# Performance work log

Measured on AMD Instinct MI355X. Metric: run time of the kernel, lower is better.

Reference implementation:

```python
import jax, jax.numpy as jnp
import numpy as np

NUM_CAPSULE = 10
DIM_CAPSULE = 16
NUM_ROUTING = 3
EPS = 1e-7  # tf.keras.backend.epsilon()


def squash(v, axis=-1):
    s2 = jnp.sum(jnp.square(v), axis=axis, keepdims=True)
    scale = s2 / (1.0 + s2) / jnp.sqrt(s2 + EPS)
    return scale * v


def setup_inputs() -> dict:
    key = jax.random.key(0)
    k1, k2 = jax.random.split(key)
    B, in_dim = 16384, 2048
    inputs = jax.random.normal(k1, (B, in_dim), dtype=jnp.float32)
    # glorot-uniform-ish scale for the kernel
    limit = np.sqrt(6.0 / (in_dim + NUM_CAPSULE * DIM_CAPSULE)).astype(np.float32)
    kernel = jax.random.uniform(k2, (in_dim, NUM_CAPSULE * DIM_CAPSULE),
                                dtype=jnp.float32, minval=-limit, maxval=limit)
    return {"inputs": inputs, "kernel": kernel}


def reference(inputs, kernel):
    B = inputs.shape[0]
    # [B, in_dim] @ [in_dim, nc*dc] -> [B, nc, dc]
    inputs_hat = (inputs @ kernel).reshape(B, NUM_CAPSULE, DIM_CAPSULE)
    b = jnp.zeros((B, NUM_CAPSULE, 1), dtype=inputs.dtype)
    outputs = None
    for _ in range(NUM_ROUTING):
        c = jax.nn.softmax(b, axis=1)                      # [B, nc, 1]
        s = jnp.sum(c * inputs_hat, axis=1, keepdims=True)  # [B, 1, dc]
        outputs = squash(s)                                 # [B, 1, dc]
        # matmul(inputs_hat, outputs, transpose_b=True) -> [B, nc, 1]
        b = b + jnp.einsum('bnd,bd->bn', inputs_hat, outputs[:, 0, :])[:, :, None]
    return outputs[:, 0, :]  # [B, dc]
```

## Files before the change

kernel.cpp:

```cpp
#include <hip/hip_runtime.h>

typedef unsigned int u32;
typedef unsigned short u16;
typedef __attribute__((ext_vector_type(8))) __bf16 bf16x8;
typedef __attribute__((ext_vector_type(4))) float f32x4;

#define N_CAP 10
#define D_CAP 16
#define NN 160
#define KK 2048
#define BM 64
#define NSTEPS 64
#define THREADS 704
#define HAT_STRIDE 165
#define BSTEP 20480
#define ATILE 8192
#define NBUF 4

__device__ __align__(16) unsigned char Wpack_g[NSTEPS * BSTEP];

__device__ __forceinline__ u32 pack_hi(float f0, float f1) {
  return __builtin_amdgcn_perm(__builtin_bit_cast(u32, f1),
                               __builtin_bit_cast(u32, f0), 0x07060302u);
}
__device__ __forceinline__ float hi_part(float f) {
  u32 u = __builtin_bit_cast(u32, f) & 0xFFFF0000u;
  return __builtin_bit_cast(float, u);
}
union U4B8 { uint4 u; bf16x8 b; };

__device__ __forceinline__ void split2(const float4& x, const float4& y,
                                       bf16x8& h, bf16x8& l) {
  U4B8 hh, ll;
  hh.u.x = pack_hi(x.x, x.y); hh.u.y = pack_hi(x.z, x.w);
  hh.u.z = pack_hi(y.x, y.y); hh.u.w = pack_hi(y.z, y.w);
  float l0 = x.x - hi_part(x.x), l1 = x.y - hi_part(x.y);
  float l2 = x.z - hi_part(x.z), l3 = x.w - hi_part(x.w);
  float l4 = y.x - hi_part(y.x), l5 = y.y - hi_part(y.y);
  float l6 = y.z - hi_part(y.z), l7 = y.w - hi_part(y.w);
  ll.u.x = pack_hi(l0, l1); ll.u.y = pack_hi(l2, l3);
  ll.u.z = pack_hi(l4, l5); ll.u.w = pack_hi(l6, l7);
  h = hh.b; l = ll.b;
}

__device__ __forceinline__ void mfma12(bf16x8 ah0, bf16x8 al0, bf16x8 ah1,
                                       bf16x8 al1, bf16x8 bh0, bf16x8 bh1,
                                       bf16x8 bl0, bf16x8 bl1, f32x4& a00,
                                       f32x4& a01, f32x4& a10, f32x4& a11) {
  a00 = __builtin_amdgcn_mfma_f32_16x16x32_bf16(ah0, bh0, a00, 0, 0, 0);
  a00 = __builtin_amdgcn_mfma_f32_16x16x32_bf16(ah0, bl0, a00, 0, 0, 0);
  a00 = __builtin_amdgcn_mfma_f32_16x16x32_bf16(al0, bh0, a00, 0, 0, 0);
  a01 = __builtin_amdgcn_mfma_f32_16x16x32_bf16(ah0, bh1, a01, 0, 0, 0);
  a01 = __builtin_amdgcn_mfma_f32_16x16x32_bf16(ah0, bl1, a01, 0, 0, 0);
  a01 = __builtin_amdgcn_mfma_f32_16x16x32_bf16(al0, bh1, a01, 0, 0, 0);
  a10 = __builtin_amdgcn_mfma_f32_16x16x32_bf16(ah1, bh0, a10, 0, 0, 0);
  a10 = __builtin_amdgcn_mfma_f32_16x16x32_bf16(ah1, bl0, a10, 0, 0, 0);
  a10 = __builtin_amdgcn_mfma_f32_16x16x32_bf16(al1, bh0, a10, 0, 0, 0);
  a11 = __builtin_amdgcn_mfma_f32_16x16x32_bf16(ah1, bh1, a11, 0, 0, 0);
  a11 = __builtin_amdgcn_mfma_f32_16x16x32_bf16(ah1, bl1, a11, 0, 0, 0);
  a11 = __builtin_amdgcn_mfma_f32_16x16x32_bf16(al1, bh1, a11, 0, 0, 0);
}

__global__ void pack_w(const float* __restrict__ W) {
  const int tid = blockIdx.x * 256 + threadIdx.x;
  if (tid >= NSTEPS * 4 * 5 * 64) return;
  const int lane = tid & 63;
  const int rest = tid >> 6;
  const int wjp = rest % 5;
  const int rest2 = rest / 5;
  const int v = rest2 & 3;
  const int s = rest2 >> 2;
  const int col = 32 * wjp + 16 * (v & 1) + (lane & 15);
  const int kb = 32 * s + 8 * (lane >> 4);
  u32 r[4];
#pragma unroll
  for (int jj = 0; jj < 4; ++jj) {
    float x0 = W[(size_t)(kb + 2 * jj) * NN + col];
    float x1 = W[(size_t)(kb + 2 * jj + 1) * NN + col];
    if (v >= 2) { x0 -= hi_part(x0); x1 -= hi_part(x1); }
    r[jj] = pack_hi(x0, x1);
  }
  uint4 o; o.x = r[0]; o.y = r[1]; o.z = r[2]; o.w = r[3];
  *(uint4*)(Wpack_g + (size_t)tid * 16) = o;
}

#define GLOAD(gp, lp) __builtin_amdgcn_global_load_lds( \
    (const __attribute__((address_space(1))) u32*)(gp), \
    (__attribute__((address_space(3))) u32*)(lp), 16, 0, 0)
#define BARRIER() asm volatile("s_barrier" ::: "memory")

__global__ __launch_bounds__(THREADS, 1) void capsule_fused(
    const float* __restrict__ X, float* __restrict__ out) {
  __shared__ __align__(16) char AsA[NBUF * ATILE];
  __shared__ __align__(16) char AsB[NBUF * BSTEP];
  __shared__ __align__(16) float hat[BM * HAT_STRIDE];

  const int t = threadIdx.x;
  const int rbase = blockIdx.x * BM;
  const int lane = t & 63;
  const int w = t >> 6;

  if (w == 10) {
    const float* g0 = X + (size_t)(rbase + (lane >> 3)) * KK
                        + (size_t)(((lane & 7) ^ (lane >> 3)) * 4);
    const unsigned char* gw0 = Wpack_g + (size_t)lane * 16;
#define STAGE(S, BV) do {                                         \
    const float* ga_ = g0 + (size_t)(S) * 32;                     \
    char* la_ = AsA + (BV) * ATILE;                               \
    GLOAD(ga_,           la_);                                    \
    GLOAD(ga_ +  8 * KK, la_ + 1024);                             \
    GLOAD(ga_ + 16 * KK, la_ + 2048);                             \
    GLOAD(ga_ + 24 * KK, la_ + 3072);                             \
    GLOAD(ga_ + 32 * KK, la_ + 4096);                             \
    GLOAD(ga_ + 40 * KK, la_ + 5120);                             \
    GLOAD(ga_ + 48 * KK, la_ + 6144);                             \
    GLOAD(ga_ + 56 * KK, la_ + 7168);                             \
    const unsigned char* gw_ = gw0 + (size_t)(S) * BSTEP;         \
    char* lw_ = AsB + (BV) * BSTEP;                               \
    _Pragma("unroll")                                             \
    for (int c_ = 0; c_ < 20; ++c_)                               \
      GLOAD(gw_ + c_ * 1024, lw_ + c_ * 1024);                    \
  } while (0)
    STAGE(0, 0);
    STAGE(1, 1);
    asm volatile("s_waitcnt vmcnt(0)" ::: "memory");
    BARRIER();
    STAGE(2, 2);
    BARRIER();
#pragma unroll 1
    for (int i = 0; i < NSTEPS; ++i) {
      if (i + 3 < NSTEPS) {
        STAGE(i + 3, (i + 3) & 3);
        asm volatile("s_waitcnt vmcnt(28)" ::: "memory");
      } else {
        asm volatile("s_waitcnt vmcnt(0)" ::: "memory");
      }
      BARRIER();
    }
#undef STAGE
  } else {
    const int wip = (w >= 5) ? 1 : 0;
    const int wjp = w - 5 * wip;
    const int l15 = lane & 15;
    const int q = lane >> 4;
    const int r0 = 32 * wip + l15;
    const int r1 = r0 + 16;
    const int c0 = 2 * q, c1 = 2 * q + 1;
    const int o00 = (r0 >> 3) * 1024 + (r0 & 7) * 128 + ((c0 ^ (r0 & 7)) << 4);
    const int o01 = (r0 >> 3) * 1024 + (r0 & 7) * 128 + ((c1 ^ (r0 & 7)) << 4);
    const int o10 = (r1 >> 3) * 1024 + (r1 & 7) * 128 + ((c0 ^ (r1 & 7)) << 4);
    const int o11 = (r1 >> 3) * 1024 + (r1 & 7) * 128 + ((c1 ^ (r1 & 7)) << 4);
    const int ob = wjp * 1024 + lane * 16;

    f32x4 acc00 = {0.f,0.f,0.f,0.f}, acc01 = {0.f,0.f,0.f,0.f};
    f32x4 acc10 = {0.f,0.f,0.f,0.f}, acc11 = {0.f,0.f,0.f,0.f};

    float4 A00a, A01a, A10a, A11a, A00b, A01b, A10b, A11b;
    bf16x8 Bh0a, Bh1a, Bl0a, Bl1a, Bh0b, Bh1b, Bl0b, Bl1b;

#define READSET(SFX, SLOT) do {                                   \
    const char* ca_ = AsA + (SLOT) * ATILE;                       \
    const char* cb_ = AsB + (SLOT) * BSTEP + ob;                  \
    A00##SFX = *(const float4*)(ca_ + o00);                       \
    A01##SFX = *(const float4*)(ca_ + o01);                       \
    A10##SFX = *(const float4*)(ca_ + o10);                       \
    A11##SFX = *(const float4*)(ca_ + o11);                       \
    Bh0##SFX = *(const bf16x8*)(cb_);                             \
    Bh1##SFX = *(const bf16x8*)(cb_ + 5120);                      \
    Bl0##SFX = *(const bf16x8*)(cb_ + 10240);                     \
    Bl1##SFX = *(const bf16x8*)(cb_ + 15360);                     \
  } while (0)

#define COMPUTE(SFX) do {                                         \
    bf16x8 ah0, al0, ah1, al1;                                    \
    split2(A00##SFX, A01##SFX, ah0, al0);                         \
    split2(A10##SFX, A11##SFX, ah1, al1);                         \
    __builtin_amdgcn_s_setprio(1);                                \
    mfma12(ah0, al0, ah1, al1, Bh0##SFX, Bh1##SFX, Bl0##SFX,      \
           Bl1##SFX, acc00, acc01, acc10, acc11);                 \
    __builtin_amdgcn_s_setprio(0);                                \
  } while (0)

    BARRIER();
    READSET(a, 0);
    BARRIER();
    int ni = 1;
#pragma unroll 1
    for (int ii = 0; ii < NSTEPS / 2; ++ii) {
      READSET(b, ni);
      ni = (ni + 1) & 3;
      COMPUTE(a);
      BARRIER();
      if (ii != NSTEPS / 2 - 1) {
        READSET(a, ni);
        ni = (ni + 1) & 3;
      }
      COMPUTE(b);
      BARRIER();
    }
#undef READSET
#undef COMPUTE

#pragma unroll
    for (int r = 0; r < 4; ++r) {
      const int rowb = 32 * wip + 4 * q + r;
      const int colb = 32 * wjp + l15;
      hat[rowb * HAT_STRIDE + colb]             = acc00[r];
      hat[rowb * HAT_STRIDE + colb + 16]        = acc01[r];
      hat[(rowb + 16) * HAT_STRIDE + colb]      = acc10[r];
      hat[(rowb + 16) * HAT_STRIDE + colb + 16] = acc11[r];
    }
  }
  __syncthreads();

  if (t < BM * 8) {
    const int r = t >> 3;
    const int d0 = t & 7;
    float h0[N_CAP], h1[N_CAP];
#pragma unroll
    for (int n = 0; n < N_CAP; ++n) {
      h0[n] = hat[r * HAT_STRIDE + n * D_CAP + d0];
      h1[n] = hat[r * HAT_STRIDE + n * D_CAP + d0 + 8];
    }
    float bb[N_CAP];
#pragma unroll
    for (int n = 0; n < N_CAP; ++n) bb[n] = 0.f;
    float v0 = 0.f, v1 = 0.f;
#pragma unroll
    for (int it = 0; it < 3; ++it) {
      float mx = bb[0];
#pragma unroll
      for (int n = 1; n < N_CAP; ++n) mx = fmaxf(mx, bb[n]);
      float c[N_CAP], se = 0.f;
#pragma unroll
      for (int n = 0; n < N_CAP; ++n) { c[n] = __expf(bb[n] - mx); se += c[n]; }
      const float inv = 1.f / se;
      float s0 = 0.f, s1 = 0.f;
#pragma unroll
      for (int n = 0; n < N_CAP; ++n) { s0 += c[n] * h0[n]; s1 += c[n] * h1[n]; }
      s0 *= inv; s1 *= inv;
      float s2 = s0 * s0 + s1 * s1;
      s2 += __shfl_xor(s2, 1);
      s2 += __shfl_xor(s2, 2);
      s2 += __shfl_xor(s2, 4);
      const float scale = s2 / ((1.f + s2) * sqrtf(s2 + 1e-7f));
      v0 = scale * s0; v1 = scale * s1;
      if (it < 2) {
#pragma unroll
        for (int n = 0; n < N_CAP; ++n) {
          float dd = h0[n] * v0 + h1[n] * v1;
          dd += __shfl_xor(dd, 1);
          dd += __shfl_xor(dd, 2);
          dd += __shfl_xor(dd, 4);
          bb[n] += dd;
        }
      }
    }
    out[(size_t)(rbase + r) * D_CAP + d0] = v0;
    out[(size_t)(rbase + r) * D_CAP + d0 + 8] = v1;
  }
}

extern "C" void kernel_launch(void* const* d_in, const int* in_sizes, int n_in,
                              void* d_out, int out_size, void* d_ws, size_t ws_size,
                              hipStream_t stream) {
  const float* X = (const float*)d_in[0];
  const float* W = (const float*)d_in[1];
  if (n_in >= 2 && in_sizes[0] == KK * NN) {
    X = (const float*)d_in[1];
    W = (const float*)d_in[0];
  }
  (void)d_ws; (void)ws_size; (void)out_size;
  pack_w<<<(NSTEPS * 4 * 5 * 64 + 255) / 256, 256, 0, stream>>>(W);
  capsule_fused<<<16384 / BM, THREADS, 0, stream>>>(X, (float*)d_out);
}
```

Measured before the change: 202.1 us.

## Load packed weight fragments directly from global into registers, dropping LDS staging

The packed bf16 hi/lo weight tiles are no longer staged through LDS by the loader wave. Each compute wave now reads its 64-byte per-lane fragment straight from global memory (L2-resident) with a one-step register prefetch. The pack layout is reordered so each lane's four fragments are contiguous, and the loader's vmcnt wait drops to match fewer in-flight loads. This frees about 80KB of LDS and shrinks loader traffic, but exposes compute waves to global-load latency and adds vector registers.

```diff
diff --git a/kernel.cpp b/kernel.cpp
--- a/kernel.cpp
+++ b/kernel.cpp
@@ -44,32 +44,33 @@
 }
 
 __device__ __forceinline__ void mfma12(bf16x8 ah0, bf16x8 al0, bf16x8 ah1,
-                                       bf16x8 al1, bf16x8 bh0, bf16x8 bh1,
-                                       bf16x8 bl0, bf16x8 bl1, f32x4& a00,
-                                       f32x4& a01, f32x4& a10, f32x4& a11) {
-  a00 = __builtin_amdgcn_mfma_f32_16x16x32_bf16(ah0, bh0, a00, 0, 0, 0);
-  a00 = __builtin_amdgcn_mfma_f32_16x16x32_bf16(ah0, bl0, a00, 0, 0, 0);
-  a00 = __builtin_amdgcn_mfma_f32_16x16x32_bf16(al0, bh0, a00, 0, 0, 0);
-  a01 = __builtin_amdgcn_mfma_f32_16x16x32_bf16(ah0, bh1, a01, 0, 0, 0);
-  a01 = __builtin_amdgcn_mfma_f32_16x16x32_bf16(ah0, bl1, a01, 0, 0, 0);
-  a01 = __builtin_amdgcn_mfma_f32_16x16x32_bf16(al0, bh1, a01, 0, 0, 0);
-  a10 = __builtin_amdgcn_mfma_f32_16x16x32_bf16(ah1, bh0, a10, 0, 0, 0);
-  a10 = __builtin_amdgcn_mfma_f32_16x16x32_bf16(ah1, bl0, a10, 0, 0, 0);
-  a10 = __builtin_amdgcn_mfma_f32_16x16x32_bf16(al1, bh0, a10, 0, 0, 0);
-  a11 = __builtin_amdgcn_mfma_f32_16x16x32_bf16(ah1, bh1, a11, 0, 0, 0);
-  a11 = __builtin_amdgcn_mfma_f32_16x16x32_bf16(ah1, bl1, a11, 0, 0, 0);
-  a11 = __builtin_amdgcn_mfma_f32_16x16x32_bf16(al1, bh1, a11, 0, 0, 0);
+                                       bf16x8 al1, uint4 b0, uint4 b1, uint4 b2,
+                                       uint4 b3, f32x4& a00, f32x4& a01,
+                                       f32x4& a10, f32x4& a11) {
+  U4B8 u0, u1, u2, u3;
+  u0.u = b0; u1.u = b1; u2.u = b2; u3.u = b3;
+  a00 = __builtin_amdgcn_mfma_f32_16x16x32_bf16(ah0, u0.b, a00, 0, 0, 0);
+  a00 = __builtin_amdgcn_mfma_f32_16x16x32_bf16(ah0, u2.b, a00, 0, 0, 0);
+  a00 = __builtin_amdgcn_mfma_f32_16x16x32_bf16(al0, u0.b, a00, 0, 0, 0);
+  a01 = __builtin_amdgcn_mfma_f32_16x16x32_bf16(ah0, u1.b, a01, 0, 0, 0);
+  a01 = __builtin_amdgcn_mfma_f32_16x16x32_bf16(ah0, u3.b, a01, 0, 0, 0);
+  a01 = __builtin_amdgcn_mfma_f32_16x16x32_bf16(al0, u1.b, a01, 0, 0, 0);
+  a10 = __builtin_amdgcn_mfma_f32_16x16x32_bf16(ah1, u0.b, a10, 0, 0, 0);
+  a10 = __builtin_amdgcn_mfma_f32_16x16x32_bf16(ah1, u2.b, a10, 0, 0, 0);
+  a10 = __builtin_amdgcn_mfma_f32_16x16x32_bf16(al1, u0.b, a10, 0, 0, 0);
+  a11 = __builtin_amdgcn_mfma_f32_16x16x32_bf16(ah1, u1.b, a11, 0, 0, 0);
+  a11 = __builtin_amdgcn_mfma_f32_16x16x32_bf16(ah1, u3.b, a11, 0, 0, 0);
+  a11 = __builtin_amdgcn_mfma_f32_16x16x32_bf16(al1, u1.b, a11, 0, 0, 0);
 }
 
 __global__ void pack_w(const float* __restrict__ W) {
   const int tid = blockIdx.x * 256 + threadIdx.x;
-  if (tid >= NSTEPS * 4 * 5 * 64) return;
-  const int lane = tid & 63;
-  const int rest = tid >> 6;
-  const int wjp = rest % 5;
-  const int rest2 = rest / 5;
-  const int v = rest2 & 3;
-  const int s = rest2 >> 2;
+  if (tid >= NSTEPS * 5 * 64 * 4) return;
+  const int v = tid & 3;
+  const int lane = (tid >> 2) & 63;
+  const int sw = tid >> 8;
+  const int wjp = sw % 5;
+  const int s = sw / 5;
   const int col = 32 * wjp + 16 * (v & 1) + (lane & 15);
   const int kb = 32 * s + 8 * (lane >> 4);
   u32 r[4];
@@ -92,7 +93,6 @@
 __global__ __launch_bounds__(THREADS, 1) void capsule_fused(
     const float* __restrict__ X, float* __restrict__ out) {
   __shared__ __align__(16) char AsA[NBUF * ATILE];
-  __shared__ __align__(16) char AsB[NBUF * BSTEP];
   __shared__ __align__(16) float hat[BM * HAT_STRIDE];
 
   const int t = threadIdx.x;
@@ -103,7 +103,6 @@
   if (w == 10) {
     const float* g0 = X + (size_t)(rbase + (lane >> 3)) * KK
                         + (size_t)(((lane & 7) ^ (lane >> 3)) * 4);
-    const unsigned char* gw0 = Wpack_g + (size_t)lane * 16;
 #define STAGE(S, BV) do {                                         \
     const float* ga_ = g0 + (size_t)(S) * 32;                     \
     char* la_ = AsA + (BV) * ATILE;                               \
@@ -115,11 +114,6 @@
     GLOAD(ga_ + 40 * KK, la_ + 5120);                             \
     GLOAD(ga_ + 48 * KK, la_ + 6144);                             \
     GLOAD(ga_ + 56 * KK, la_ + 7168);                             \
-    const unsigned char* gw_ = gw0 + (size_t)(S) * BSTEP;         \
-    char* lw_ = AsB + (BV) * BSTEP;                               \
-    _Pragma("unroll")                                             \
-    for (int c_ = 0; c_ < 20; ++c_)                               \
-      GLOAD(gw_ + c_ * 1024, lw_ + c_ * 1024);                    \
   } while (0)
     STAGE(0, 0);
     STAGE(1, 1);
@@ -131,7 +125,7 @@
     for (int i = 0; i < NSTEPS; ++i) {
       if (i + 3 < NSTEPS) {
         STAGE(i + 3, (i + 3) & 3);
-        asm volatile("s_waitcnt vmcnt(28)" ::: "memory");
+        asm volatile("s_waitcnt vmcnt(8)" ::: "memory");
       } else {
         asm volatile("s_waitcnt vmcnt(0)" ::: "memory");
       }
@@ -150,55 +144,59 @@
     const int o01 = (r0 >> 3) * 1024 + (r0 & 7) * 128 + ((c1 ^ (r0 & 7)) << 4);
     const int o10 = (r1 >> 3) * 1024 + (r1 & 7) * 128 + ((c0 ^ (r1 & 7)) << 4);
     const int o11 = (r1 >> 3) * 1024 + (r1 & 7) * 128 + ((c1 ^ (r1 & 7)) << 4);
-    const int ob = wjp * 1024 + lane * 16;
+    const unsigned char* pB = Wpack_g + ((size_t)wjp * 64 + lane) * 64;
 
     f32x4 acc00 = {0.f,0.f,0.f,0.f}, acc01 = {0.f,0.f,0.f,0.f};
     f32x4 acc10 = {0.f,0.f,0.f,0.f}, acc11 = {0.f,0.f,0.f,0.f};
 
     float4 A00a, A01a, A10a, A11a, A00b, A01b, A10b, A11b;
-    bf16x8 Bh0a, Bh1a, Bl0a, Bl1a, Bh0b, Bh1b, Bl0b, Bl1b;
+    uint4 Bc0, Bc1, Bc2, Bc3, Bn0, Bn1, Bn2, Bn3;
 
 #define READSET(SFX, SLOT) do {                                   \
     const char* ca_ = AsA + (SLOT) * ATILE;                       \
-    const char* cb_ = AsB + (SLOT) * BSTEP + ob;                  \
     A00##SFX = *(const float4*)(ca_ + o00);                       \
     A01##SFX = *(const float4*)(ca_ + o01);                       \
     A10##SFX = *(const float4*)(ca_ + o10);                       \
     A11##SFX = *(const float4*)(ca_ + o11);                       \
-    Bh0##SFX = *(const bf16x8*)(cb_);                             \
-    Bh1##SFX = *(const bf16x8*)(cb_ + 5120);                      \
-    Bl0##SFX = *(const bf16x8*)(cb_ + 10240);                     \
-    Bl1##SFX = *(const bf16x8*)(cb_ + 15360);                     \
-  } while (0)
-
-#define COMPUTE(SFX) do {                                         \
+  } while (0)
+
+#define BLOADC(P0, P1, P2, P3, S) do {                            \
+    const uint4* bp_ = (const uint4*)(pB + (size_t)(S) * BSTEP);  \
+    P0 = bp_[0]; P1 = bp_[1]; P2 = bp_[2]; P3 = bp_[3];           \
+  } while (0)
+
+#define COMPUTE(SFX, P0, P1, P2, P3) do {                         \
     bf16x8 ah0, al0, ah1, al1;                                    \
     split2(A00##SFX, A01##SFX, ah0, al0);                         \
     split2(A10##SFX, A11##SFX, ah1, al1);                         \
     __builtin_amdgcn_s_setprio(1);                                \
-    mfma12(ah0, al0, ah1, al1, Bh0##SFX, Bh1##SFX, Bl0##SFX,      \
-           Bl1##SFX, acc00, acc01, acc10, acc11);                 \
+    mfma12(ah0, al0, ah1, al1, P0, P1, P2, P3,                    \
+           acc00, acc01, acc10, acc11);                           \
     __builtin_amdgcn_s_setprio(0);                                \
   } while (0)
 
+    BLOADC(Bc0, Bc1, Bc2, Bc3, 0);
     BARRIER();
     READSET(a, 0);
     BARRIER();
     int ni = 1;
 #pragma unroll 1
     for (int ii = 0; ii < NSTEPS / 2; ++ii) {
+      BLOADC(Bn0, Bn1, Bn2, Bn3, 2 * ii + 1);
       READSET(b, ni);
       ni = (ni + 1) & 3;
-      COMPUTE(a);
+      COMPUTE(a, Bc0, Bc1, Bc2, Bc3);
       BARRIER();
+      BLOADC(Bc0, Bc1, Bc2, Bc3, (2 * ii + 2) & (NSTEPS - 1));
       if (ii != NSTEPS / 2 - 1) {
         READSET(a, ni);
         ni = (ni + 1) & 3;
       }
-      COMPUTE(b);
+      COMPUTE(b, Bn0, Bn1, Bn2, Bn3);
       BARRIER();
     }
 #undef READSET
+#undef BLOADC
 #undef COMPUTE
 
 #pragma unroll
@@ -271,6 +269,6 @@
     W = (const float*)d_in[0];
   }
   (void)d_ws; (void)ws_size; (void)out_size;
-  pack_w<<<(NSTEPS * 4 * 5 * 64 + 255) / 256, 256, 0, stream>>>(W);
+  pack_w<<<(NSTEPS * 5 * 64 * 4 + 255) / 256, 256, 0, stream>>>(W);
   capsule_fused<<<16384 / BM, THREADS, 0, stream>>>(X, (float*)d_out);
 }
```

Result: slower. 212.6 us (+5.2%).
